# Kernel tuning notes

Measured on AMD Instinct MI355X. Metric: run time of the kernel, lower is better.

Reference implementation:

```python
import jax, jax.numpy as jnp
import numpy as np

DIM = 1024
HEADS = 16
HEAD_DIM = DIM // HEADS
FFN = 4096
EPS = 1e-6


def layernorm(x, a, b):
    # torch: mean, std (unbiased, ddof=1), divide by (std + eps)
    mean = jnp.mean(x, axis=-1, keepdims=True)
    std = jnp.std(x, axis=-1, keepdims=True, ddof=1)
    return a * (x - mean) / (std + EPS) + b


def setup_inputs() -> dict:
    key = jax.random.key(0)
    ks = jax.random.split(key, 8)
    B, S = 2, 2048
    x = jax.random.normal(ks[0], (B, S, DIM), dtype=jnp.float32)
    mask = jnp.zeros((1, 1, S, S), dtype=jnp.float32)
    sc = 0.02
    wq = jax.random.normal(ks[1], (DIM, DIM), jnp.float32) * sc
    wk = jax.random.normal(ks[2], (DIM, DIM), jnp.float32) * sc
    wv = jax.random.normal(ks[3], (DIM, DIM), jnp.float32) * sc
    wo = jax.random.normal(ks[4], (DIM, DIM), jnp.float32) * sc
    w1 = jax.random.normal(ks[5], (FFN, DIM), jnp.float32) * sc
    w2 = jax.random.normal(ks[6], (DIM, FFN), jnp.float32) * sc
    a1 = jnp.ones((DIM,), jnp.float32)
    b1 = jnp.zeros((DIM,), jnp.float32)
    a2 = jnp.ones((DIM,), jnp.float32)
    b2 = jnp.zeros((DIM,), jnp.float32)
    return {"x": x, "mask": mask, "wq": wq, "wk": wk, "wv": wv, "wo": wo,
            "w1": w1, "w2": w2, "a1": a1, "b1": b1, "a2": a2, "b2": b2}


def reference(x, mask, wq, wk, wv, wo, w1, w2, a1, b1, a2, b2):
    B, S, _ = x.shape
    # QKV projections (Linear weight is [out, in]; y = x @ W.T)
    q = (x @ wq.T).reshape(B, S, HEADS, HEAD_DIM).transpose(0, 2, 1, 3)
    k = (x @ wk.T).reshape(B, S, HEADS, HEAD_DIM).transpose(0, 2, 1, 3)
    v = (x @ wv.T).reshape(B, S, HEADS, HEAD_DIM).transpose(0, 2, 1, 3)
    scores = jnp.einsum('bhqd,bhkd->bhqk', q, k) / np.sqrt(HEAD_DIM).astype(np.float32)
    scores = scores + mask
    probs = jax.nn.softmax(scores.astype(jnp.float32), axis=-1).astype(q.dtype)
    attn = jnp.einsum('bhqk,bhkd->bhqd', probs, v)
    attn = attn.transpose(0, 2, 1, 3).reshape(B, S, DIM)
    attn_out = attn @ wo.T
    attn_x = layernorm(x + attn_out, a1, b1)
    # FFN with exact (erf) GELU, matching nn.GELU default
    h = jax.nn.gelu(attn_x @ w1.T, approximate=False)
    ffn_out = h @ w2.T
    return layernorm(attn_x + ffn_out, a2, b2)
```

## Files before the change

kernel.cpp:

```cpp
#include <hip/hip_runtime.h>
#include <math.h>

typedef __bf16 bf16x8 __attribute__((ext_vector_type(8)));
typedef float  f32x4  __attribute__((ext_vector_type(4)));
typedef unsigned short us4 __attribute__((ext_vector_type(4)));

__device__ __forceinline__ unsigned short f2bf(float f) {
    union { float f; unsigned int u; } v; v.f = f;
    return (unsigned short)((v.u + 0x7FFFu + ((v.u >> 16) & 1u)) >> 16);
}

__device__ __forceinline__ unsigned cvt_pk_bf16(float lo, float hi) {
    unsigned r;
    asm("v_cvt_pk_bf16_f32 %0, %1, %2" : "=v"(r) : "v"(lo), "v"(hi));
    return r;
}

__device__ __forceinline__ float exp2_raw(float x) {
    float r;
    asm("v_exp_f32 %0, %1" : "=v"(r) : "v"(x));
    return r;
}

__device__ __forceinline__ void gload_lds16(const unsigned short* g, unsigned short* l) {
    __builtin_amdgcn_global_load_lds((__attribute__((address_space(1))) void*)(g),
                                     (__attribute__((address_space(3))) void*)(l), 16, 0, 0);
}

__global__ __launch_bounds__(256)
void cast_kernel(const float* __restrict__ in, unsigned short* __restrict__ out, int n) {
    const int i = (blockIdx.x * 256 + threadIdx.x) * 4;
    if (i < n) {
        const float4 v = *reinterpret_cast<const float4*>(in + i);
        us4 o = { f2bf(v.x), f2bf(v.y), f2bf(v.z), f2bf(v.w) };
        *reinterpret_cast<us4*>(out + i) = o;
    }
}

template<int EPI>
__global__ __launch_bounds__(256)
void gemm_bt(const unsigned short* __restrict__ A, const unsigned short* __restrict__ B,
             void* __restrict__ Cout, int M, int N, int K) {
    __shared__ __align__(16) unsigned short lds[2][2][128 * 32];
    const int tid = threadIdx.x;
    const int l   = tid & 63;
    const int w   = tid >> 6;
    const int bm  = blockIdx.x * 128;
    const int bn  = blockIdx.y * 128;
    const int wr  = (w >> 1) * 64;
    const int wc  = (w & 1) * 64;
    const int wbase = tid & ~63;

    f32x4 acc[4][4] = {};

    auto stage = [&](int buf, int k0) {
#pragma unroll
        for (int c = 0; c < 2; ++c) {
            const int chunk = c * 256 + tid;
            const int r  = chunk >> 2;
            const int cl = (chunk & 3) ^ ((r >> 1) & 3);
            gload_lds16(A + (size_t)(bm + r) * K + k0 + cl * 8,
                        &lds[buf][0][(c * 256 + wbase) * 8]);
        }
#pragma unroll
        for (int c = 0; c < 2; ++c) {
            const int chunk = c * 256 + tid;
            const int r  = chunk >> 2;
            const int cl = (chunk & 3) ^ ((r >> 1) & 3);
            gload_lds16(B + (size_t)(bn + r) * K + k0 + cl * 8,
                        &lds[buf][1][(c * 256 + wbase) * 8]);
        }
    };

    stage(0, 0);
    int cur = 0;
    const int nk = K >> 5;
    for (int kt = 0; kt < nk; ++kt) {
        __syncthreads();
        if (kt + 1 < nk) stage(cur ^ 1, (kt + 1) << 5);
        bf16x8 af[4], bfr[4];
#pragma unroll
        for (int i = 0; i < 4; ++i) {
            const int ra = wr + i * 16 + (l & 15);
            const int ca = (l >> 4) ^ ((ra >> 1) & 3);
            af[i]  = *reinterpret_cast<const bf16x8*>(&lds[cur][0][ra * 32 + ca * 8]);
            const int rb = wc + i * 16 + (l & 15);
            const int cb = (l >> 4) ^ ((rb >> 1) & 3);
            bfr[i] = *reinterpret_cast<const bf16x8*>(&lds[cur][1][rb * 32 + cb * 8]);
        }
#pragma unroll
        for (int i = 0; i < 4; ++i)
#pragma unroll
            for (int j = 0; j < 4; ++j)
                acc[i][j] = __builtin_amdgcn_mfma_f32_16x16x32_bf16(af[i], bfr[j], acc[i][j], 0, 0, 0);
        cur ^= 1;
    }

#pragma unroll
    for (int i = 0; i < 4; ++i) {
#pragma unroll
        for (int j = 0; j < 4; ++j) {
#pragma unroll
            for (int r = 0; r < 4; ++r) {
                const int m = bm + wr + i * 16 + ((l >> 4) << 2) + r;
                const int n = bn + wc + j * 16 + (l & 15);
                const float v = acc[i][j][r];
                if (EPI == 0) {
                    ((float*)Cout)[(size_t)m * N + n] = v;
                } else if (EPI == 1) {
                    unsigned short* C = (unsigned short*)Cout;
                    const int s  = m & 2047;
                    const int bh = ((m >> 11) << 4) | ((n & 1023) >> 6);
                    const int d  = n & 63;
                    if (n < 1024)
                        C[(size_t)(bh * 2048 + s) * 64 + d] = f2bf(v * 0.18033688011112042f);
                    else if (n < 2048)
                        C[(size_t)4194304 + (size_t)(bh * 2048 + s) * 64 + d] = f2bf(v);
                    else
                        C[(size_t)8388608 + ((size_t)bh * 64 + d) * 2048 + s] = f2bf(v);
                } else {
                    const float g = 0.5f * v * (1.0f + erff(v * 0.70710678118654752f));
                    ((unsigned short*)Cout)[(size_t)m * N + n] = f2bf(g);
                }
            }
        }
    }
}

__global__ __launch_bounds__(256)
void attn_kernel(const unsigned short* __restrict__ Q, const unsigned short* __restrict__ Kb,
                 const unsigned short* __restrict__ Vt, unsigned short* __restrict__ out) {
    __shared__ __align__(16) unsigned short kld[2][64 * 64];
    __shared__ __align__(16) unsigned short vld[2][64 * 64];
    __shared__ __align__(16) unsigned short plds[4][2][16][72];
    const int tid = threadIdx.x;
    const int l   = tid & 63;
    const int w   = tid >> 6;
    const int g   = l >> 4;
    const int q15 = l & 15;
    const int bh  = blockIdx.x & 31;
    const int qt  = blockIdx.x >> 5;
    const int q0  = qt * 128 + w * 32;
    const size_t base = (size_t)bh * 2048 * 64;

    bf16x8 qa[2][2];
#pragma unroll
    for (int qg = 0; qg < 2; ++qg) {
        const unsigned short* qp = Q + base + (size_t)(q0 + qg * 16 + q15) * 64 + g * 8;
        qa[qg][0] = *reinterpret_cast<const bf16x8*>(qp);
        qa[qg][1] = *reinterpret_cast<const bf16x8*>(qp + 32);
    }

    f32x4 oacc[2][4] = {};
    float mrun[2] = { -1e30f, -1e30f };
    float lsum[2] = { 0.f, 0.f };

    auto stage = [&](int buf, int k0) {
        const int wb = tid & ~63;
#pragma unroll
        for (int it = 0; it < 2; ++it) {
            const int ci = it * 256 + tid;
            const int r  = ci >> 3;
            const int cs = (ci & 7) ^ (r & 7);
            gload_lds16(Kb + base + (size_t)(k0 + r) * 64 + cs * 8,
                        &kld[buf][(it * 256 + wb) * 8]);
        }
#pragma unroll
        for (int it = 0; it < 2; ++it) {
            const int ci = it * 256 + tid;
            const int r  = ci >> 3;
            const int cs = (ci & 7) ^ (r & 7);
            gload_lds16(Vt + base + (size_t)r * 2048 + k0 + cs * 8,
                        &vld[buf][(it * 256 + wb) * 8]);
        }
    };

    stage(0, 0);
    int cur = 0;
    for (int t = 0; t < 32; ++t) {
        __syncthreads();
        if (t + 1 < 32) stage(cur ^ 1, (t + 1) * 64);

        bf16x8 kf[4][2];
#pragma unroll
        for (int ks = 0; ks < 4; ++ks) {
            const int row = ks * 16 + q15;
            const int sw  = row & 7;
            kf[ks][0] = *reinterpret_cast<const bf16x8*>(&kld[cur][row * 64 + ((g    ) ^ sw) * 8]);
            kf[ks][1] = *reinterpret_cast<const bf16x8*>(&kld[cur][row * 64 + ((4 + g) ^ sw) * 8]);
        }
        f32x4 sac[2][4];
#pragma unroll
        for (int qg = 0; qg < 2; ++qg)
#pragma unroll
            for (int ks = 0; ks < 4; ++ks) {
                f32x4 z = { 0.f, 0.f, 0.f, 0.f };
                z = __builtin_amdgcn_mfma_f32_16x16x32_bf16(kf[ks][0], qa[qg][0], z, 0, 0, 0);
                z = __builtin_amdgcn_mfma_f32_16x16x32_bf16(kf[ks][1], qa[qg][1], z, 0, 0, 0);
                sac[qg][ks] = z;
            }

#pragma unroll
        for (int qg = 0; qg < 2; ++qg) {
            float tm = fmaxf(fmaxf(sac[qg][0][0], sac[qg][0][1]), fmaxf(sac[qg][0][2], sac[qg][0][3]));
#pragma unroll
            for (int ks = 1; ks < 4; ++ks) {
                const float a = fmaxf(sac[qg][ks][0], sac[qg][ks][1]);
                const float b = fmaxf(sac[qg][ks][2], sac[qg][ks][3]);
                tm = fmaxf(tm, fmaxf(a, b));
            }
            tm = fmaxf(tm, __shfl_xor(tm, 16));
            tm = fmaxf(tm, __shfl_xor(tm, 32));
            const bool skip = __all(tm <= mrun[qg] + 8.0f);
            const float mnew = skip ? mrun[qg] : fmaxf(mrun[qg], tm);
            float ps = 0.f;
#pragma unroll
            for (int ks = 0; ks < 4; ++ks) {
                const float p0 = exp2_raw(sac[qg][ks][0] - mnew);
                const float p1 = exp2_raw(sac[qg][ks][1] - mnew);
                const float p2 = exp2_raw(sac[qg][ks][2] - mnew);
                const float p3 = exp2_raw(sac[qg][ks][3] - mnew);
                ps += (p0 + p1) + (p2 + p3);
                uint2 pk;
                pk.x = cvt_pk_bf16(p0, p1);
                pk.y = cvt_pk_bf16(p2, p3);
                *reinterpret_cast<uint2*>(&plds[w][qg][q15][ks * 16 + g * 4]) = pk;
            }
            ps += __shfl_xor(ps, 16);
            ps += __shfl_xor(ps, 32);
            if (skip) {
                lsum[qg] += ps;
            } else {
                const float sc = exp2_raw(mrun[qg] - mnew);
                float scr[4];
#pragma unroll
                for (int r = 0; r < 4; ++r) scr[r] = __shfl(sc, (l & 48) | (g * 4 + r));
#pragma unroll
                for (int j = 0; j < 4; ++j)
#pragma unroll
                    for (int r = 0; r < 4; ++r) oacc[qg][j][r] *= scr[r];
                lsum[qg] = lsum[qg] * sc + ps;
                mrun[qg] = mnew;
            }
        }

        bf16x8 pa[2][2];
#pragma unroll
        for (int qg = 0; qg < 2; ++qg) {
            pa[qg][0] = *reinterpret_cast<const bf16x8*>(&plds[w][qg][q15][g * 8]);
            pa[qg][1] = *reinterpret_cast<const bf16x8*>(&plds[w][qg][q15][32 + g * 8]);
        }
#pragma unroll
        for (int j = 0; j < 4; ++j) {
            const int row = j * 16 + q15;
            const int sw  = row & 7;
            const bf16x8 v0 = *reinterpret_cast<const bf16x8*>(&vld[cur][row * 64 + ((g    ) ^ sw) * 8]);
            const bf16x8 v1 = *reinterpret_cast<const bf16x8*>(&vld[cur][row * 64 + ((4 + g) ^ sw) * 8]);
#pragma unroll
            for (int qg = 0; qg < 2; ++qg) {
                oacc[qg][j] = __builtin_amdgcn_mfma_f32_16x16x32_bf16(pa[qg][0], v0, oacc[qg][j], 0, 0, 0);
                oacc[qg][j] = __builtin_amdgcn_mfma_f32_16x16x32_bf16(pa[qg][1], v1, oacc[qg][j], 0, 0, 0);
            }
        }
        cur ^= 1;
    }

    const int b = bh >> 4, h = bh & 15;
#pragma unroll
    for (int qg = 0; qg < 2; ++qg) {
        const float li = 1.f / lsum[qg];
        float lir[4];
#pragma unroll
        for (int r = 0; r < 4; ++r) lir[r] = __shfl(li, (l & 48) | (g * 4 + r));
#pragma unroll
        for (int j = 0; j < 4; ++j)
#pragma unroll
            for (int r = 0; r < 4; ++r) {
                const int q = q0 + qg * 16 + g * 4 + r;
                out[(size_t)(b * 2048 + q) * 1024 + h * 64 + j * 16 + q15] = f2bf(oacc[qg][j][r] * lir[r]);
            }
    }
}

__global__ __launch_bounds__(256)
void ln_res(const float* __restrict__ X, const float* __restrict__ R,
            const float* __restrict__ gamma, const float* __restrict__ beta,
            float* __restrict__ o32, unsigned short* __restrict__ o16) {
    __shared__ float red[4];
    const int t = threadIdx.x;
    const size_t row = blockIdx.x;
    const float4 a = *reinterpret_cast<const float4*>(X + row * 1024 + t * 4);
    const float4 b = *reinterpret_cast<const float4*>(R + row * 1024 + t * 4);
    float v0 = a.x + b.x, v1 = a.y + b.y, v2 = a.z + b.z, v3 = a.w + b.w;
    float s = v0 + v1 + v2 + v3;
#pragma unroll
    for (int o = 1; o < 64; o <<= 1) s += __shfl_xor(s, o);
    if ((t & 63) == 0) red[t >> 6] = s;
    __syncthreads();
    const float mean = (red[0] + red[1] + red[2] + red[3]) * (1.f / 1024.f);
    v0 -= mean; v1 -= mean; v2 -= mean; v3 -= mean;
    float q = v0 * v0 + v1 * v1 + v2 * v2 + v3 * v3;
#pragma unroll
    for (int o = 1; o < 64; o <<= 1) q += __shfl_xor(q, o);
    __syncthreads();
    if ((t & 63) == 0) red[t >> 6] = q;
    __syncthreads();
    const float var = (red[0] + red[1] + red[2] + red[3]) * (1.f / 1023.f);
    const float inv = 1.f / (sqrtf(var) + 1e-6f);
    const float4 g  = *reinterpret_cast<const float4*>(gamma + t * 4);
    const float4 be = *reinterpret_cast<const float4*>(beta + t * 4);
    const float y0 = g.x * v0 * inv + be.x;
    const float y1 = g.y * v1 * inv + be.y;
    const float y2 = g.z * v2 * inv + be.z;
    const float y3 = g.w * v3 * inv + be.w;
    float4 o4; o4.x = y0; o4.y = y1; o4.z = y2; o4.w = y3;
    *reinterpret_cast<float4*>(o32 + row * 1024 + t * 4) = o4;
    if (o16) {
        us4 ob = { f2bf(y0), f2bf(y1), f2bf(y2), f2bf(y3) };
        *reinterpret_cast<us4*>(o16 + row * 1024 + t * 4) = ob;
    }
}

extern "C" void kernel_launch(void* const* d_in, const int* in_sizes, int n_in,
                              void* d_out, int out_size, void* d_ws, size_t ws_size,
                              hipStream_t stream) {
    const float* x  = (const float*)d_in[0];
    const float* wq = (const float*)d_in[2];
    const float* wk = (const float*)d_in[3];
    const float* wv = (const float*)d_in[4];
    const float* wo = (const float*)d_in[5];
    const float* w1 = (const float*)d_in[6];
    const float* w2 = (const float*)d_in[7];
    const float* a1 = (const float*)d_in[8];
    const float* b1 = (const float*)d_in[9];
    const float* a2 = (const float*)d_in[10];
    const float* b2 = (const float*)d_in[11];

    char* ws = (char*)d_ws;
    const size_t MB = 1024 * 1024;
    unsigned short* xb      = (unsigned short*)(ws);
    unsigned short* wqkv    = (unsigned short*)(ws + 8  * MB);
    unsigned short* wob     = (unsigned short*)(ws + 14 * MB);
    unsigned short* hbuf    = (unsigned short*)(ws);
    unsigned short* w1b     = (unsigned short*)(ws + 32 * MB);
    unsigned short* w2b     = (unsigned short*)(ws + 40 * MB);
    unsigned short* qkv     = (unsigned short*)(ws + 48 * MB);
    unsigned short* attn    = (unsigned short*)(ws + 72 * MB);
    float*          attn_o  = (float*)(ws + 80 * MB);
    float*          attn_x  = (float*)(ws + 96 * MB);
    unsigned short* attn_xb = (unsigned short*)(ws + 112 * MB);

    cast_kernel<<<4096, 256, 0, stream>>>(x,  xb,   4194304);
    cast_kernel<<<1024, 256, 0, stream>>>(wq, wqkv,            1048576);
    cast_kernel<<<1024, 256, 0, stream>>>(wk, wqkv + 1048576,  1048576);
    cast_kernel<<<1024, 256, 0, stream>>>(wv, wqkv + 2097152,  1048576);
    cast_kernel<<<1024, 256, 0, stream>>>(wo, wob, 1048576);
    cast_kernel<<<4096, 256, 0, stream>>>(w1, w1b, 4194304);
    cast_kernel<<<4096, 256, 0, stream>>>(w2, w2b, 4194304);

    gemm_bt<1><<<dim3(32, 24), 256, 0, stream>>>(xb, wqkv, qkv, 4096, 3072, 1024);
    attn_kernel<<<512, 256, 0, stream>>>(qkv, qkv + 4194304, qkv + 8388608, attn);
    gemm_bt<0><<<dim3(32, 8), 256, 0, stream>>>(attn, wob, attn_o, 4096, 1024, 1024);
    ln_res<<<4096, 256, 0, stream>>>(x, attn_o, a1, b1, attn_x, attn_xb);
    gemm_bt<2><<<dim3(32, 32), 256, 0, stream>>>(attn_xb, w1b, hbuf, 4096, 4096, 1024);
    gemm_bt<0><<<dim3(32, 8), 256, 0, stream>>>(hbuf, w2b, attn_o, 4096, 1024, 4096);
    ln_res<<<4096, 256, 0, stream>>>(attn_x, attn_o, a2, b2, (float*)d_out, nullptr);
}
```

Measured before the change: 286.2 us.

## Fuse casts, swizzle GEMM tiles, split-K FFN2, MFMA rowsum in attention

Replaces the seven cast launches with one combined kernel. The GEMM now remaps workgroups through an XCD-aware swizzle for L2 locality. The FFN down-projection (K=4096) is split four ways, with bf16 partials summed inside the layernorm kernel, and projection outputs are stored as bf16 rather than fp32. In attention, the per-row softmax sum comes from an extra MFMA against a ones vector instead of shuffles. Storing partials in bf16 lowers residual precision, and split-K adds partial-buffer traffic.

```diff
diff --git a/kernel.cpp b/kernel.cpp
--- a/kernel.cpp
+++ b/kernel.cpp
@@ -9,44 +9,61 @@
     union { float f; unsigned int u; } v; v.f = f;
     return (unsigned short)((v.u + 0x7FFFu + ((v.u >> 16) & 1u)) >> 16);
 }
-
+__device__ __forceinline__ float bf2f(unsigned short u) {
+    union { unsigned int i; float f; } c; c.i = (unsigned)u << 16;
+    return c.f;
+}
 __device__ __forceinline__ unsigned cvt_pk_bf16(float lo, float hi) {
     unsigned r;
     asm("v_cvt_pk_bf16_f32 %0, %1, %2" : "=v"(r) : "v"(lo), "v"(hi));
     return r;
 }
-
 __device__ __forceinline__ float exp2_raw(float x) {
     float r;
     asm("v_exp_f32 %0, %1" : "=v"(r) : "v"(x));
     return r;
 }
-
 __device__ __forceinline__ void gload_lds16(const unsigned short* g, unsigned short* l) {
     __builtin_amdgcn_global_load_lds((__attribute__((address_space(1))) void*)(g),
                                      (__attribute__((address_space(3))) void*)(l), 16, 0, 0);
 }
 
 __global__ __launch_bounds__(256)
-void cast_kernel(const float* __restrict__ in, unsigned short* __restrict__ out, int n) {
-    const int i = (blockIdx.x * 256 + threadIdx.x) * 4;
-    if (i < n) {
-        const float4 v = *reinterpret_cast<const float4*>(in + i);
-        us4 o = { f2bf(v.x), f2bf(v.y), f2bf(v.z), f2bf(v.w) };
-        *reinterpret_cast<us4*>(out + i) = o;
-    }
+void cast_all(const float* __restrict__ x, const float* __restrict__ wq,
+              const float* __restrict__ wk, const float* __restrict__ wv,
+              const float* __restrict__ wo, const float* __restrict__ w1,
+              const float* __restrict__ w2,
+              unsigned short* __restrict__ xb, unsigned short* __restrict__ wqkv,
+              unsigned short* __restrict__ wob, unsigned short* __restrict__ w1b,
+              unsigned short* __restrict__ w2b) {
+    const int b = blockIdx.x;
+    const float* src; unsigned short* dst; int off;
+    if      (b <  4096) { src = x;  dst = xb;             off = b;         }
+    else if (b <  5120) { src = wq; dst = wqkv;           off = b - 4096;  }
+    else if (b <  6144) { src = wk; dst = wqkv + 1048576; off = b - 5120;  }
+    else if (b <  7168) { src = wv; dst = wqkv + 2097152; off = b - 6144;  }
+    else if (b <  8192) { src = wo; dst = wob;            off = b - 7168;  }
+    else if (b < 12288) { src = w1; dst = w1b;            off = b - 8192;  }
+    else                { src = w2; dst = w2b;            off = b - 12288; }
+    const int i = off * 1024 + threadIdx.x * 4;
+    const float4 v = *reinterpret_cast<const float4*>(src + i);
+    us4 o = { f2bf(v.x), f2bf(v.y), f2bf(v.z), f2bf(v.w) };
+    *reinterpret_cast<us4*>(dst + i) = o;
 }
 
 template<int EPI>
 __global__ __launch_bounds__(256)
 void gemm_bt(const unsigned short* __restrict__ A, const unsigned short* __restrict__ B,
-             void* __restrict__ Cout, int M, int N, int K) {
+             void* __restrict__ Cout, int M, int N, int Kstride, int Kc, int NBY) {
     __shared__ __align__(16) unsigned short lds[2][2][128 * 32];
     const int tid = threadIdx.x;
     const int l   = tid & 63;
     const int w   = tid >> 6;
-    const int bm  = blockIdx.x * 128;
-    const int bn  = blockIdx.y * 128;
+    const int wg  = blockIdx.x;
+    const int swz = (wg & 7) * (gridDim.x >> 3) + (wg >> 3);
+    const int bm  = (swz / NBY) * 128;
+    const int bn  = (swz % NBY) * 128;
+    const int kbase = blockIdx.y * Kc;
     const int wr  = (w >> 1) * 64;
     const int wc  = (w & 1) * 64;
     const int wbase = tid & ~63;
@@ -59,7 +76,7 @@
             const int chunk = c * 256 + tid;
             const int r  = chunk >> 2;
             const int cl = (chunk & 3) ^ ((r >> 1) & 3);
-            gload_lds16(A + (size_t)(bm + r) * K + k0 + cl * 8,
+            gload_lds16(A + (size_t)(bm + r) * Kstride + kbase + k0 + cl * 8,
                         &lds[buf][0][(c * 256 + wbase) * 8]);
         }
 #pragma unroll
@@ -67,14 +84,14 @@
             const int chunk = c * 256 + tid;
             const int r  = chunk >> 2;
             const int cl = (chunk & 3) ^ ((r >> 1) & 3);
-            gload_lds16(B + (size_t)(bn + r) * K + k0 + cl * 8,
+            gload_lds16(B + (size_t)(bn + r) * Kstride + kbase + k0 + cl * 8,
                         &lds[buf][1][(c * 256 + wbase) * 8]);
         }
     };
 
     stage(0, 0);
     int cur = 0;
-    const int nk = K >> 5;
+    const int nk = Kc >> 5;
     for (int kt = 0; kt < nk; ++kt) {
         __syncthreads();
         if (kt + 1 < nk) stage(cur ^ 1, (kt + 1) << 5);
@@ -105,9 +122,7 @@
                 const int m = bm + wr + i * 16 + ((l >> 4) << 2) + r;
                 const int n = bn + wc + j * 16 + (l & 15);
                 const float v = acc[i][j][r];
-                if (EPI == 0) {
-                    ((float*)Cout)[(size_t)m * N + n] = v;
-                } else if (EPI == 1) {
+                if (EPI == 1) {
                     unsigned short* C = (unsigned short*)Cout;
                     const int s  = m & 2047;
                     const int bh = ((m >> 11) << 4) | ((n & 1023) >> 6);
@@ -118,9 +133,11 @@
                         C[(size_t)4194304 + (size_t)(bh * 2048 + s) * 64 + d] = f2bf(v);
                     else
                         C[(size_t)8388608 + ((size_t)bh * 64 + d) * 2048 + s] = f2bf(v);
+                } else if (EPI == 2) {
+                    const float gl = 0.5f * v * (1.0f + erff(v * 0.70710678118654752f));
+                    ((unsigned short*)Cout)[(size_t)m * N + n] = f2bf(gl);
                 } else {
-                    const float g = 0.5f * v * (1.0f + erff(v * 0.70710678118654752f));
-                    ((unsigned short*)Cout)[(size_t)m * N + n] = f2bf(g);
+                    ((unsigned short*)Cout)[(size_t)blockIdx.y * M * N + (size_t)m * N + n] = f2bf(v);
                 }
             }
         }
@@ -151,9 +168,17 @@
         qa[qg][1] = *reinterpret_cast<const bf16x8*>(qp + 32);
     }
 
-    f32x4 oacc[2][4] = {};
+    bf16x8 ones;
+    {
+        us4 o1 = { 0x3F80, 0x3F80, 0x3F80, 0x3F80 };
+        bf16x8 t;
+        *reinterpret_cast<us4*>(&t) = o1;
+        *(reinterpret_cast<us4*>(&t) + 1) = o1;
+        ones = t;
+    }
+
+    f32x4 oacc[2][5] = {};
     float mrun[2] = { -1e30f, -1e30f };
-    float lsum[2] = { 0.f, 0.f };
 
     auto stage = [&](int buf, int k0) {
         const int wb = tid & ~63;
@@ -213,33 +238,26 @@
             tm = fmaxf(tm, __shfl_xor(tm, 32));
             const bool skip = __all(tm <= mrun[qg] + 8.0f);
             const float mnew = skip ? mrun[qg] : fmaxf(mrun[qg], tm);
-            float ps = 0.f;
 #pragma unroll
             for (int ks = 0; ks < 4; ++ks) {
                 const float p0 = exp2_raw(sac[qg][ks][0] - mnew);
                 const float p1 = exp2_raw(sac[qg][ks][1] - mnew);
                 const float p2 = exp2_raw(sac[qg][ks][2] - mnew);
                 const float p3 = exp2_raw(sac[qg][ks][3] - mnew);
-                ps += (p0 + p1) + (p2 + p3);
                 uint2 pk;
                 pk.x = cvt_pk_bf16(p0, p1);
                 pk.y = cvt_pk_bf16(p2, p3);
                 *reinterpret_cast<uint2*>(&plds[w][qg][q15][ks * 16 + g * 4]) = pk;
             }
-            ps += __shfl_xor(ps, 16);
-            ps += __shfl_xor(ps, 32);
-            if (skip) {
-                lsum[qg] += ps;
-            } else {
+            if (!skip) {
                 const float sc = exp2_raw(mrun[qg] - mnew);
                 float scr[4];
 #pragma unroll
                 for (int r = 0; r < 4; ++r) scr[r] = __shfl(sc, (l & 48) | (g * 4 + r));
 #pragma unroll
-                for (int j = 0; j < 4; ++j)
+                for (int j = 0; j < 5; ++j)
 #pragma unroll
                     for (int r = 0; r < 4; ++r) oacc[qg][j][r] *= scr[r];
-                lsum[qg] = lsum[qg] * sc + ps;
                 mrun[qg] = mnew;
             }
         }
@@ -262,36 +280,42 @@
                 oacc[qg][j] = __builtin_amdgcn_mfma_f32_16x16x32_bf16(pa[qg][1], v1, oacc[qg][j], 0, 0, 0);
             }
         }
+#pragma unroll
+        for (int qg = 0; qg < 2; ++qg) {
+            oacc[qg][4] = __builtin_amdgcn_mfma_f32_16x16x32_bf16(pa[qg][0], ones, oacc[qg][4], 0, 0, 0);
+            oacc[qg][4] = __builtin_amdgcn_mfma_f32_16x16x32_bf16(pa[qg][1], ones, oacc[qg][4], 0, 0, 0);
+        }
         cur ^= 1;
     }
 
     const int b = bh >> 4, h = bh & 15;
 #pragma unroll
-    for (int qg = 0; qg < 2; ++qg) {
-        const float li = 1.f / lsum[qg];
-        float lir[4];
-#pragma unroll
-        for (int r = 0; r < 4; ++r) lir[r] = __shfl(li, (l & 48) | (g * 4 + r));
-#pragma unroll
-        for (int j = 0; j < 4; ++j)
-#pragma unroll
-            for (int r = 0; r < 4; ++r) {
-                const int q = q0 + qg * 16 + g * 4 + r;
-                out[(size_t)(b * 2048 + q) * 1024 + h * 64 + j * 16 + q15] = f2bf(oacc[qg][j][r] * lir[r]);
-            }
-    }
-}
-
+    for (int qg = 0; qg < 2; ++qg)
+#pragma unroll
+        for (int r = 0; r < 4; ++r) {
+            const float inv = 1.f / oacc[qg][4][r];
+            const int q = q0 + qg * 16 + g * 4 + r;
+#pragma unroll
+            for (int j = 0; j < 4; ++j)
+                out[(size_t)(b * 2048 + q) * 1024 + h * 64 + j * 16 + q15] = f2bf(oacc[qg][j][r] * inv);
+        }
+}
+
+template<int NP>
 __global__ __launch_bounds__(256)
-void ln_res(const float* __restrict__ X, const float* __restrict__ R,
+void ln_res(const float* __restrict__ X, const unsigned short* __restrict__ P,
             const float* __restrict__ gamma, const float* __restrict__ beta,
             float* __restrict__ o32, unsigned short* __restrict__ o16) {
     __shared__ float red[4];
     const int t = threadIdx.x;
     const size_t row = blockIdx.x;
     const float4 a = *reinterpret_cast<const float4*>(X + row * 1024 + t * 4);
-    const float4 b = *reinterpret_cast<const float4*>(R + row * 1024 + t * 4);
-    float v0 = a.x + b.x, v1 = a.y + b.y, v2 = a.z + b.z, v3 = a.w + b.w;
+    float v0 = a.x, v1 = a.y, v2 = a.z, v3 = a.w;
+#pragma unroll
+    for (int p = 0; p < NP; ++p) {
+        const us4 rr = *reinterpret_cast<const us4*>(P + (size_t)p * 4194304 + row * 1024 + t * 4);
+        v0 += bf2f(rr.x); v1 += bf2f(rr.y); v2 += bf2f(rr.z); v3 += bf2f(rr.w);
+    }
     float s = v0 + v1 + v2 + v3;
 #pragma unroll
     for (int o = 1; o < 64; o <<= 1) s += __shfl_xor(s, o);
@@ -346,23 +370,17 @@
     unsigned short* w2b     = (unsigned short*)(ws + 40 * MB);
     unsigned short* qkv     = (unsigned short*)(ws + 48 * MB);
     unsigned short* attn    = (unsigned short*)(ws + 72 * MB);
-    float*          attn_o  = (float*)(ws + 80 * MB);
+    unsigned short* ffn2p   = (unsigned short*)(ws + 48 * MB);
+    unsigned short* projp   = (unsigned short*)(ws + 80 * MB);
     float*          attn_x  = (float*)(ws + 96 * MB);
     unsigned short* attn_xb = (unsigned short*)(ws + 112 * MB);
 
-    cast_kernel<<<4096, 256, 0, stream>>>(x,  xb,   4194304);
-    cast_kernel<<<1024, 256, 0, stream>>>(wq, wqkv,            1048576);
-    cast_kernel<<<1024, 256, 0, stream>>>(wk, wqkv + 1048576,  1048576);
-    cast_kernel<<<1024, 256, 0, stream>>>(wv, wqkv + 2097152,  1048576);
-    cast_kernel<<<1024, 256, 0, stream>>>(wo, wob, 1048576);
-    cast_kernel<<<4096, 256, 0, stream>>>(w1, w1b, 4194304);
-    cast_kernel<<<4096, 256, 0, stream>>>(w2, w2b, 4194304);
-
-    gemm_bt<1><<<dim3(32, 24), 256, 0, stream>>>(xb, wqkv, qkv, 4096, 3072, 1024);
+    cast_all<<<16384, 256, 0, stream>>>(x, wq, wk, wv, wo, w1, w2, xb, wqkv, wob, w1b, w2b);
+    gemm_bt<1><<<dim3(768, 1), 256, 0, stream>>>(xb, wqkv, qkv, 4096, 3072, 1024, 1024, 24);
     attn_kernel<<<512, 256, 0, stream>>>(qkv, qkv + 4194304, qkv + 8388608, attn);
-    gemm_bt<0><<<dim3(32, 8), 256, 0, stream>>>(attn, wob, attn_o, 4096, 1024, 1024);
-    ln_res<<<4096, 256, 0, stream>>>(x, attn_o, a1, b1, attn_x, attn_xb);
-    gemm_bt<2><<<dim3(32, 32), 256, 0, stream>>>(attn_xb, w1b, hbuf, 4096, 4096, 1024);
-    gemm_bt<0><<<dim3(32, 8), 256, 0, stream>>>(hbuf, w2b, attn_o, 4096, 1024, 4096);
-    ln_res<<<4096, 256, 0, stream>>>(attn_x, attn_o, a2, b2, (float*)d_out, nullptr);
-}
+    gemm_bt<3><<<dim3(256, 1), 256, 0, stream>>>(attn, wob, projp, 4096, 1024, 1024, 1024, 8);
+    ln_res<1><<<4096, 256, 0, stream>>>(x, projp, a1, b1, attn_x, attn_xb);
+    gemm_bt<2><<<dim3(1024, 1), 256, 0, stream>>>(attn_xb, w1b, hbuf, 4096, 4096, 1024, 1024, 32);
+    gemm_bt<3><<<dim3(256, 4), 256, 0, stream>>>(hbuf, w2b, ffn2p, 4096, 1024, 4096, 1024, 8);
+    ln_res<4><<<4096, 256, 0, stream>>>(attn_x, ffn2p, a2, b2, (float*)d_out, nullptr);
+}
```

Result: faster. 268.9 us (-6.0%).
